# Optimization experiments

Hardware: AMD Instinct MI355X
Metric: run time of the kernel (lower is better)

Reference implementation:

```python
import jax, jax.numpy as jnp
import numpy as np

B, D, K = 16384, 4096, 14
EPS = 1e-12  # torch F.normalize eps


def _normalize(x):
    n = jnp.sqrt(jnp.sum(x * x, axis=-1, keepdims=True))
    return x / jnp.maximum(n, EPS)


def setup_inputs() -> dict:
    key = jax.random.key(0)
    ks = jax.random.split(key, 9)
    image_feat = jax.random.normal(ks[0], (B, D), dtype=jnp.float32)
    text_feat = jax.random.normal(ks[1], (B, D), dtype=jnp.float32)
    disease_labels = jax.random.randint(ks[2], (B, K), 0, 2, dtype=jnp.int32)
    # nn.Linear default init: U(-1/sqrt(D), 1/sqrt(D))
    lim = 1.0 / np.sqrt(D)
    Wv = jax.random.uniform(ks[3], (D, D), jnp.float32, -lim, lim)
    bv = jax.random.uniform(ks[4], (D,), jnp.float32, -lim, lim)
    Wt = jax.random.uniform(ks[5], (D, D), jnp.float32, -lim, lim)
    bt = jax.random.uniform(ks[6], (D,), jnp.float32, -lim, lim)
    prototypes = jax.random.normal(ks[7], (K, D), dtype=jnp.float32) * 0.02
    cooccur = np.eye(K, dtype=np.float32)
    for i, j in [(1, 3), (0, 9), (7, 9)]:
        cooccur[i, j] = 0.7
        cooccur[j, i] = 0.7
    cooccurrence = jnp.asarray(cooccur)
    return {
        "image_feat": image_feat, "text_feat": text_feat,
        "disease_labels": disease_labels,
        "Wv": Wv, "bv": bv, "Wt": Wt, "bt": bt,
        "prototypes": prototypes, "cooccurrence": cooccurrence,
    }


def reference(image_feat, text_feat, disease_labels, Wv, bv, Wt, bt, prototypes, cooccurrence):
    labels_f = disease_labels.astype(jnp.float32)  # [B, K]
    v = _normalize(image_feat @ Wv.T + bv)          # [B, D]
    t = _normalize(text_feat @ Wt.T + bt)           # [B, D]
    p = _normalize(prototypes)                      # [K, D]
    v_sim = v @ p.T                                 # [B, K]
    t_sim = t @ p.T                                 # [B, K]
    # Coalition value is linear in the mask and the sampled coalitions differ
    # only at index i, so every Monte Carlo marginal equals this closed form
    # exactly (randomness cancels in value_with - value_without).
    shapley = 0.5 * (v_sim + t_sim) * labels_f      # [B, K]
    batch_cooccur = (labels_f.T @ labels_f) / labels_f.shape[0]  # [K, K]
    learned = jax.nn.sigmoid(cooccurrence)
    cooccur_loss = jnp.mean((learned - jax.lax.stop_gradient(batch_cooccur)) ** 2)
    return shapley, prototypes, cooccur_loss
```

## Files before the change

kernel.cpp:

```cpp
#include <hip/hip_runtime.h>

typedef __bf16 bf16x8 __attribute__((ext_vector_type(8)));
typedef float f32x4 __attribute__((ext_vector_type(4)));
typedef unsigned short u16;
typedef unsigned int u32;

#define D_DIM 4096
#define B_ROWS 16384
#define K_CLS 14
#define M_TOT 32768

__device__ __forceinline__ u32 f2bf(float f) {
    u32 u = __float_as_uint(f);
    return (u + 0x7FFFu + ((u >> 16) & 1u)) >> 16;
}
__device__ __forceinline__ float bfl(u32 u) { return __uint_as_float(u << 16); }
__device__ __forceinline__ float bfh(u32 u) { return __uint_as_float(u & 0xFFFF0000u); }

typedef __attribute__((address_space(3))) void lds_void;
typedef __attribute__((address_space(1))) void glb_void;

__device__ __forceinline__ void g2lds16(const void* g, void* l) {
    __builtin_amdgcn_global_load_lds(
        reinterpret_cast<glb_void*>(reinterpret_cast<uintptr_t>(g)),
        reinterpret_cast<lds_void*>(reinterpret_cast<uintptr_t>(l)),
        16, 0, 0);
}

__global__ void cast_bf16(const float* __restrict__ src, u16* __restrict__ dst, int n4) {
    int i = blockIdx.x * blockDim.x + threadIdx.x;
    int stride = gridDim.x * blockDim.x;
    for (; i < n4; i += stride) {
        float4 a = ((const float4*)src)[i];
        uint2 o;
        o.x = f2bf(a.x) | (f2bf(a.y) << 16);
        o.y = f2bf(a.z) | (f2bf(a.w) << 16);
        ((uint2*)dst)[i] = o;
    }
}

__global__ void proto_norm(const float* __restrict__ P, u16* __restrict__ pTbf,
                           float* __restrict__ outProto) {
    const int k = blockIdx.x;
    const int tid = threadIdx.x;
    float ss = 0.f;
    for (int d = tid; d < D_DIM; d += 256) {
        float v = P[k * D_DIM + d];
        ss += v * v;
    }
    for (int off = 32; off; off >>= 1) ss += __shfl_down(ss, off);
    __shared__ float red[4];
    if ((tid & 63) == 0) red[tid >> 6] = ss;
    __syncthreads();
    float tot = red[0] + red[1] + red[2] + red[3];
    float inv = 1.0f / fmaxf(sqrtf(tot), 1e-12f);
    for (int d = tid; d < D_DIM; d += 256) {
        float v = P[k * D_DIM + d];
        outProto[k * D_DIM + d] = v;
        pTbf[(size_t)d * 16 + k] = (u16)f2bf(v * inv);
    }
}

__global__ void cooccur_bc(const int* __restrict__ L, float* __restrict__ bc) {
    const int i = blockIdx.x / K_CLS, j = blockIdx.x % K_CLS;
    int s = 0;
    for (int b = threadIdx.x; b < B_ROWS; b += 256)
        s += L[b * K_CLS + i] * L[b * K_CLS + j];
    for (int off = 32; off; off >>= 1) s += __shfl_down(s, off);
    __shared__ int red[4];
    if ((threadIdx.x & 63) == 0) red[threadIdx.x >> 6] = s;
    __syncthreads();
    if (threadIdx.x == 0)
        bc[blockIdx.x] = (float)(red[0] + red[1] + red[2] + red[3]) / (float)B_ROWS;
}

__global__ void cooccur_loss(const float* __restrict__ C, const float* __restrict__ bc,
                             float* __restrict__ out) {
    const int t = threadIdx.x;
    float d2 = 0.f;
    if (t < K_CLS * K_CLS) {
        float s = 1.0f / (1.0f + expf(-C[t]));
        float d = s - bc[t];
        d2 = d * d;
    }
    for (int off = 32; off; off >>= 1) d2 += __shfl_down(d2, off);
    __shared__ float red[4];
    if ((t & 63) == 0) red[t >> 6] = d2;
    __syncthreads();
    if (t == 0) out[0] = (red[0] + red[1] + red[2] + red[3]) / (float)(K_CLS * K_CLS);
}

__global__ __launch_bounds__(256) void gemm_bt(
    const u16* __restrict__ Xbf,
    const u16* __restrict__ Wbf,
    const float* __restrict__ bv, const float* __restrict__ bt,
    u16* __restrict__ Ybf)
{
    __shared__ __align__(16) u16 As[128 * 32];
    __shared__ __align__(16) u16 Bs[128 * 32];

    const int tid = threadIdx.x;
    const int wave = tid >> 6, lane = tid & 63;
    const int bn0 = blockIdx.x * 128;
    const int bm0 = blockIdx.y * 128;
    const int half = (bm0 >= B_ROWS) ? 1 : 0;
    const u16* Wsel = Wbf + (size_t)half * D_DIM * D_DIM;
    const float* bias = half ? bt : bv;

    const int srA = lane >> 2;
    const int sc  = (lane & 3) * 8;
    const int g0 = wave * 2, g1 = wave * 2 + 1;
    const u16* Ag = Xbf + (size_t)bm0 * D_DIM;
    const u16* Bg = Wsel + (size_t)bn0 * D_DIM;
    const u16* ga0 = Ag + (size_t)(g0 * 16 + srA) * D_DIM + sc;
    const u16* ga1 = Ag + (size_t)(g1 * 16 + srA) * D_DIM + sc;
    const u16* gb0 = Bg + (size_t)(g0 * 16 + srA) * D_DIM + sc;
    const u16* gb1 = Bg + (size_t)(g1 * 16 + srA) * D_DIM + sc;
    u16* la0 = &As[g0 * 512]; u16* la1 = &As[g1 * 512];
    u16* lb0 = &Bs[g0 * 512]; u16* lb1 = &Bs[g1 * 512];

    const int waveM = wave >> 1, waveN = wave & 1;
    const int mlane = lane & 15, quad = lane >> 4;
    const u16* Ar = &As[(waveM * 64 + mlane) * 32 + quad * 8];
    const u16* Br = &Bs[(waveN * 64 + mlane) * 32 + quad * 8];

    f32x4 acc[4][4] = {};

    for (int k0 = 0; k0 < D_DIM; k0 += 32) {
        __syncthreads();
        g2lds16(ga0 + k0, la0);
        g2lds16(ga1 + k0, la1);
        g2lds16(gb0 + k0, lb0);
        g2lds16(gb1 + k0, lb1);
        __syncthreads();
        bf16x8 a[4], b[4];
#pragma unroll
        for (int mi = 0; mi < 4; mi++) a[mi] = *(const bf16x8*)(Ar + mi * 16 * 32);
#pragma unroll
        for (int ni = 0; ni < 4; ni++) b[ni] = *(const bf16x8*)(Br + ni * 16 * 32);
#pragma unroll
        for (int mi = 0; mi < 4; mi++)
#pragma unroll
            for (int ni = 0; ni < 4; ni++)
                acc[mi][ni] = __builtin_amdgcn_mfma_f32_16x16x32_bf16(
                    a[mi], b[ni], acc[mi][ni], 0, 0, 0);
    }

#pragma unroll
    for (int ni = 0; ni < 4; ni++) {
        const int col = bn0 + waveN * 64 + ni * 16 + mlane;
        const float bcol = bias[col];
#pragma unroll
        for (int mi = 0; mi < 4; mi++) {
            f32x4 v = acc[mi][ni];
#pragma unroll
            for (int r = 0; r < 4; r++) {
                const int row = bm0 + waveM * 64 + mi * 16 + quad * 4 + r;
                Ybf[(size_t)row * D_DIM + col] = (u16)f2bf(v[r] + bcol);
            }
        }
    }
}

__global__ __launch_bounds__(256) void simproj(
    const u16* __restrict__ Ybf, const u16* __restrict__ pTbf,
    float* __restrict__ sim)
{
    const int tid = threadIdx.x;
    const int wave = tid >> 6, lane = tid & 63;
    const int r0 = blockIdx.x * 16 + wave * 4;
    const u16* Y0 = Ybf + (size_t)r0 * D_DIM;

    float acc[4][15];
#pragma unroll
    for (int r = 0; r < 4; r++)
#pragma unroll
        for (int k = 0; k < 15; k++) acc[r][k] = 0.f;

#pragma unroll 2
    for (int i = 0; i < 64; i++) {
        const int d = lane + i * 64;
        const uint4* pq = (const uint4*)(pTbf + (size_t)d * 16);
        const uint4 q0 = pq[0], q1 = pq[1];
        const float p[14] = { bfl(q0.x), bfh(q0.x), bfl(q0.y), bfh(q0.y),
                              bfl(q0.z), bfh(q0.z), bfl(q0.w), bfh(q0.w),
                              bfl(q1.x), bfh(q1.x), bfl(q1.y), bfh(q1.y),
                              bfl(q1.z), bfh(q1.z) };
#pragma unroll
        for (int r = 0; r < 4; r++) {
            const float yv = bfl((u32)Y0[(size_t)r * D_DIM + d]);
            acc[r][14] += yv * yv;
#pragma unroll
            for (int k = 0; k < 14; k++) acc[r][k] += yv * p[k];
        }
    }
#pragma unroll
    for (int r = 0; r < 4; r++)
#pragma unroll
        for (int k = 0; k < 15; k++) {
            float v = acc[r][k];
            v += __shfl_xor(v, 1);  v += __shfl_xor(v, 2);  v += __shfl_xor(v, 4);
            v += __shfl_xor(v, 8);  v += __shfl_xor(v, 16); v += __shfl_xor(v, 32);
            acc[r][k] = v;
        }
    if (lane == 0) {
#pragma unroll
        for (int r = 0; r < 4; r++) {
            const float inv = 1.0f / fmaxf(sqrtf(acc[r][14]), 1e-12f);
#pragma unroll
            for (int k = 0; k < 14; k++)
                sim[(size_t)(r0 + r) * K_CLS + k] = acc[r][k] * inv;
        }
    }
}

__global__ void finalize(const float* __restrict__ sim, const int* __restrict__ L,
                         float* __restrict__ out) {
    const int t = blockIdx.x * 256 + threadIdx.x;
    if (t >= B_ROWS * K_CLS) return;
    out[t] = 0.5f * (sim[t] + sim[t + B_ROWS * K_CLS]) * (float)L[t];
}

extern "C" void kernel_launch(void* const* d_in, const int* in_sizes, int n_in,
                              void* d_out, int out_size, void* d_ws, size_t ws_size,
                              hipStream_t stream) {
    const float* image  = (const float*)d_in[0];
    const float* text   = (const float*)d_in[1];
    const int*   labels = (const int*)d_in[2];
    const float* Wv     = (const float*)d_in[3];
    const float* bv     = (const float*)d_in[4];
    const float* Wt     = (const float*)d_in[5];
    const float* bt     = (const float*)d_in[6];
    const float* protos = (const float*)d_in[7];
    const float* cooc   = (const float*)d_in[8];
    float* out = (float*)d_out;

    const size_t OFF_X   = 0;
    const size_t OFF_W   = 268435456ull;
    const size_t OFF_Y   = 335544320ull;
    const size_t OFF_PT  = 603979776ull;
    const size_t OFF_SIM = 604110848ull;
    const size_t OFF_BC  = 605945856ull;
    const size_t NEED    = 605946640ull;
    if (ws_size < NEED) return;

    char* ws = (char*)d_ws;
    u16*   Xbf  = (u16*)(ws + OFF_X);
    u16*   Wbf  = (u16*)(ws + OFF_W);
    u16*   Ybf  = (u16*)(ws + OFF_Y);
    u16*   pTbf = (u16*)(ws + OFF_PT);
    float* sim  = (float*)(ws + OFF_SIM);
    float* bc   = (float*)(ws + OFF_BC);

    cast_bf16<<<4096, 256, 0, stream>>>(image, Xbf, (B_ROWS * D_DIM) / 4);
    cast_bf16<<<4096, 256, 0, stream>>>(text, Xbf + (size_t)B_ROWS * D_DIM, (B_ROWS * D_DIM) / 4);
    cast_bf16<<<2048, 256, 0, stream>>>(Wv, Wbf, (D_DIM * D_DIM) / 4);
    cast_bf16<<<2048, 256, 0, stream>>>(Wt, Wbf + (size_t)D_DIM * D_DIM, (D_DIM * D_DIM) / 4);

    proto_norm<<<K_CLS, 256, 0, stream>>>(protos, pTbf, out + B_ROWS * K_CLS);
    cooccur_bc<<<K_CLS * K_CLS, 256, 0, stream>>>(labels, bc);
    cooccur_loss<<<1, 256, 0, stream>>>(cooc, bc, out + B_ROWS * K_CLS + K_CLS * D_DIM);

    gemm_bt<<<dim3(D_DIM / 128, M_TOT / 128), 256, 0, stream>>>(Xbf, Wbf, bv, bt, Ybf);

    simproj<<<M_TOT / 16, 256, 0, stream>>>(Ybf, pTbf, sim);

    finalize<<<(B_ROWS * K_CLS + 255) / 256, 256, 0, stream>>>(sim, labels, out);
}
```

Baseline: 1.988 ms.

## Double GEMM K-tile with XOR-swizzled LDS layout and fuse cast kernels

The GEMM main loop now stages 64-wide K slices instead of 32, using an XOR swizzle on the LDS column chunk for both the global-to-LDS writes and the MFMA operand reads. This halves the number of barrier pairs per output tile and aims to avoid LDS bank conflicts on the fragment loads. The four bf16 cast launches are merged into one grid-stride kernel that picks its source by index range. LDS use per block doubles, which may affect occupancy.

```diff
diff --git a/kernel.cpp b/kernel.cpp
--- a/kernel.cpp
+++ b/kernel.cpp
@@ -9,6 +9,7 @@
 #define B_ROWS 16384
 #define K_CLS 14
 #define M_TOT 32768
+#define BK 64
 
 __device__ __forceinline__ u32 f2bf(float f) {
     u32 u = __float_as_uint(f);
@@ -27,11 +28,22 @@
         16, 0, 0);
 }
 
-__global__ void cast_bf16(const float* __restrict__ src, u16* __restrict__ dst, int n4) {
+__global__ void cast_all(const float* __restrict__ im, const float* __restrict__ tx,
+                         const float* __restrict__ wv, const float* __restrict__ wt,
+                         u16* __restrict__ dst) {
+    const int C1 = 16777216;
+    const int C2 = 33554432;
+    const int C3 = 37748736;
+    const int C4 = 41943040;
     int i = blockIdx.x * blockDim.x + threadIdx.x;
-    int stride = gridDim.x * blockDim.x;
-    for (; i < n4; i += stride) {
-        float4 a = ((const float4*)src)[i];
+    const int stride = gridDim.x * blockDim.x;
+    for (; i < C4; i += stride) {
+        const float4* s; int j;
+        if (i < C1)      { s = (const float4*)im; j = i; }
+        else if (i < C2) { s = (const float4*)tx; j = i - C1; }
+        else if (i < C3) { s = (const float4*)wv; j = i - C2; }
+        else             { s = (const float4*)wt; j = i - C3; }
+        float4 a = s[j];
         uint2 o;
         o.x = f2bf(a.x) | (f2bf(a.y) << 16);
         o.y = f2bf(a.z) | (f2bf(a.w) << 16);
@@ -96,8 +108,8 @@
     const float* __restrict__ bv, const float* __restrict__ bt,
     u16* __restrict__ Ybf)
 {
-    __shared__ __align__(16) u16 As[128 * 32];
-    __shared__ __align__(16) u16 Bs[128 * 32];
+    __shared__ __align__(16) u16 As[128 * BK];
+    __shared__ __align__(16) u16 Bs[128 * BK];
 
     const int tid = threadIdx.x;
     const int wave = tid >> 6, lane = tid & 63;
@@ -107,37 +119,55 @@
     const u16* Wsel = Wbf + (size_t)half * D_DIM * D_DIM;
     const float* bias = half ? bt : bv;
 
-    const int srA = lane >> 2;
-    const int sc  = (lane & 3) * 8;
-    const int g0 = wave * 2, g1 = wave * 2 + 1;
+    const int srow = lane >> 3;
+    const int gcol = ((lane & 7) ^ srow) * 8;
     const u16* Ag = Xbf + (size_t)bm0 * D_DIM;
     const u16* Bg = Wsel + (size_t)bn0 * D_DIM;
-    const u16* ga0 = Ag + (size_t)(g0 * 16 + srA) * D_DIM + sc;
-    const u16* ga1 = Ag + (size_t)(g1 * 16 + srA) * D_DIM + sc;
-    const u16* gb0 = Bg + (size_t)(g0 * 16 + srA) * D_DIM + sc;
-    const u16* gb1 = Bg + (size_t)(g1 * 16 + srA) * D_DIM + sc;
-    u16* la0 = &As[g0 * 512]; u16* la1 = &As[g1 * 512];
-    u16* lb0 = &Bs[g0 * 512]; u16* lb1 = &Bs[g1 * 512];
+    const u16* gA[4]; const u16* gB[4];
+    u16* lA[4]; u16* lB[4];
+#pragma unroll
+    for (int i = 0; i < 4; i++) {
+        const int g = wave * 4 + i;
+        const int row = g * 8 + srow;
+        gA[i] = Ag + (size_t)row * D_DIM + gcol;
+        gB[i] = Bg + (size_t)row * D_DIM + gcol;
+        lA[i] = &As[g * 512];
+        lB[i] = &Bs[g * 512];
+    }
 
     const int waveM = wave >> 1, waveN = wave & 1;
     const int mlane = lane & 15, quad = lane >> 4;
-    const u16* Ar = &As[(waveM * 64 + mlane) * 32 + quad * 8];
-    const u16* Br = &Bs[(waveN * 64 + mlane) * 32 + quad * 8];
+    const int sw0 = (quad ^ (mlane & 7)) * 8;
+    const int sw1 = sw0 ^ 32;
+    const u16* Ar0 = &As[(waveM * 64 + mlane) * BK + sw0];
+    const u16* Br0 = &Bs[(waveN * 64 + mlane) * BK + sw0];
+    const u16* Ar1 = &As[(waveM * 64 + mlane) * BK + sw1];
+    const u16* Br1 = &Bs[(waveN * 64 + mlane) * BK + sw1];
 
     f32x4 acc[4][4] = {};
 
-    for (int k0 = 0; k0 < D_DIM; k0 += 32) {
+    for (int k0 = 0; k0 < D_DIM; k0 += BK) {
         __syncthreads();
-        g2lds16(ga0 + k0, la0);
-        g2lds16(ga1 + k0, la1);
-        g2lds16(gb0 + k0, lb0);
-        g2lds16(gb1 + k0, lb1);
+#pragma unroll
+        for (int i = 0; i < 4; i++) g2lds16(gA[i] + k0, lA[i]);
+#pragma unroll
+        for (int i = 0; i < 4; i++) g2lds16(gB[i] + k0, lB[i]);
         __syncthreads();
         bf16x8 a[4], b[4];
 #pragma unroll
-        for (int mi = 0; mi < 4; mi++) a[mi] = *(const bf16x8*)(Ar + mi * 16 * 32);
-#pragma unroll
-        for (int ni = 0; ni < 4; ni++) b[ni] = *(const bf16x8*)(Br + ni * 16 * 32);
+        for (int mi = 0; mi < 4; mi++) a[mi] = *(const bf16x8*)(Ar0 + mi * 16 * BK);
+#pragma unroll
+        for (int ni = 0; ni < 4; ni++) b[ni] = *(const bf16x8*)(Br0 + ni * 16 * BK);
+#pragma unroll
+        for (int mi = 0; mi < 4; mi++)
+#pragma unroll
+            for (int ni = 0; ni < 4; ni++)
+                acc[mi][ni] = __builtin_amdgcn_mfma_f32_16x16x32_bf16(
+                    a[mi], b[ni], acc[mi][ni], 0, 0, 0);
+#pragma unroll
+        for (int mi = 0; mi < 4; mi++) a[mi] = *(const bf16x8*)(Ar1 + mi * 16 * BK);
+#pragma unroll
+        for (int ni = 0; ni < 4; ni++) b[ni] = *(const bf16x8*)(Br1 + ni * 16 * BK);
 #pragma unroll
         for (int mi = 0; mi < 4; mi++)
 #pragma unroll
@@ -227,9 +257,7 @@
     const float* image  = (const float*)d_in[0];
     const float* text   = (const float*)d_in[1];
     const int*   labels = (const int*)d_in[2];
-    const float* Wv     = (const float*)d_in[3];
     const float* bv     = (const float*)d_in[4];
-    const float* Wt     = (const float*)d_in[5];
     const float* bt     = (const float*)d_in[6];
     const float* protos = (const float*)d_in[7];
     const float* cooc   = (const float*)d_in[8];
@@ -252,10 +280,8 @@
     float* sim  = (float*)(ws + OFF_SIM);
     float* bc   = (float*)(ws + OFF_BC);
 
-    cast_bf16<<<4096, 256, 0, stream>>>(image, Xbf, (B_ROWS * D_DIM) / 4);
-    cast_bf16<<<4096, 256, 0, stream>>>(text, Xbf + (size_t)B_ROWS * D_DIM, (B_ROWS * D_DIM) / 4);
-    cast_bf16<<<2048, 256, 0, stream>>>(Wv, Wbf, (D_DIM * D_DIM) / 4);
-    cast_bf16<<<2048, 256, 0, stream>>>(Wt, Wbf + (size_t)D_DIM * D_DIM, (D_DIM * D_DIM) / 4);
+    cast_all<<<8192, 256, 0, stream>>>(image, text,
+                                       (const float*)d_in[3], (const float*)d_in[5], Xbf);
 
     proto_norm<<<K_CLS, 256, 0, stream>>>(protos, pTbf, out + B_ROWS * K_CLS);
     cooccur_bc<<<K_CLS * K_CLS, 256, 0, stream>>>(labels, bc);
```

Measured after the change: 2.047 ms. 1.03x slower.
